# Kernel optimization log

Hardware: AMD Instinct MI355X
Metric: run time of the kernel (lower is better)

The kernel has to match this reference:

```python
import jax, jax.numpy as jnp
import numpy as np

EMBED_DIM = 1024
NUM_HEADS = 16
HEAD_DIM = EMBED_DIM // NUM_HEADS


def setup_inputs() -> dict:
    key = jax.random.key(0)
    ks = jax.random.split(key, 9)
    B, S, D = 2, 2048, EMBED_DIM
    scale = 1.0 / np.sqrt(D)
    x = jax.random.normal(ks[0], (B, S, D), dtype=jnp.float32)
    wq = jax.random.normal(ks[1], (D, D), dtype=jnp.float32) * scale
    bq = jax.random.normal(ks[2], (D,), dtype=jnp.float32) * 0.02
    wk = jax.random.normal(ks[3], (D, D), dtype=jnp.float32) * scale
    bk = jax.random.normal(ks[4], (D,), dtype=jnp.float32) * 0.02
    wv = jax.random.normal(ks[5], (D, D), dtype=jnp.float32) * scale
    bv = jax.random.normal(ks[6], (D,), dtype=jnp.float32) * 0.02
    wo = jax.random.normal(ks[7], (D, D), dtype=jnp.float32) * scale
    bo = jax.random.normal(ks[8], (D,), dtype=jnp.float32) * 0.02
    return {"x": x, "wq": wq, "bq": bq, "wk": wk, "bk": bk,
            "wv": wv, "bv": bv, "wo": wo, "bo": bo}


def reference(x, wq, bq, wk, bk, wv, bv, wo, bo):
    B, S, D = x.shape
    H, Hd = NUM_HEADS, HEAD_DIM
    # separate QKV linears (weights stored [in, out] so x @ w)
    q = (x @ wq + bq).reshape(B, S, H, Hd).transpose(0, 2, 1, 3)  # [B,H,S,Hd]
    k = (x @ wk + bk).reshape(B, S, H, Hd).transpose(0, 2, 1, 3)
    v = (x @ wv + bv).reshape(B, S, H, Hd).transpose(0, 2, 1, 3)
    scores = jnp.einsum('bhqd,bhkd->bhqk', q, k) / jnp.sqrt(jnp.float32(Hd))
    attn = jax.nn.softmax(scores, axis=-1)
    context = jnp.einsum('bhqk,bhkd->bhqd', attn, v)
    context = context.transpose(0, 2, 1, 3).reshape(B, S, D)
    return context @ wo + bo
```

## Files before the change

kernel.cpp:

```cpp
#include <hip/hip_runtime.h>
#include <cstdint>
#include <cstddef>


typedef float floatx4 __attribute__((ext_vector_type(4)));
typedef __bf16 bf16x8 __attribute__((ext_vector_type(8)));
union ABFrag { bf16x8 v; uint4 q; unsigned short u[8]; unsigned int w[4]; };

__device__ __forceinline__ unsigned short f2bf(float f) {
    unsigned int u = __builtin_bit_cast(unsigned int, f);
    return (unsigned short)((u + 0x7FFFu + ((u >> 16) & 1u)) >> 16);
}

__device__ __forceinline__ unsigned int pkbf(float lo, float hi) {
    unsigned int a = __builtin_bit_cast(unsigned int, hi) + 0x8000u;
    unsigned int b = __builtin_bit_cast(unsigned int, lo) + 0x8000u;
    return __builtin_amdgcn_perm(a, b, 0x07060302u);
}

#if __has_builtin(__builtin_amdgcn_exp2f)
#define EXP2F(x) __builtin_amdgcn_exp2f(x)
#else
#define EXP2F(x) exp2f(x)
#endif

__device__ __forceinline__ void glds16(const void* g, void* l) {
    __builtin_amdgcn_global_load_lds(
        (const __attribute__((address_space(1))) unsigned int*)(uintptr_t)g,
        (__attribute__((address_space(3))) unsigned int*)(unsigned int)(uintptr_t)l,
        16, 0, 0);
}

__global__ void convert_x_kernel(const float* __restrict__ x,
                                 unsigned short* __restrict__ xb) {
    int i = (blockIdx.x * 256 + threadIdx.x) * 8;
    float4 a = *(const float4*)(x + i);
    float4 b = *(const float4*)(x + i + 4);
    union { unsigned short u[8]; uint4 q; } o;
    o.u[0] = f2bf(a.x); o.u[1] = f2bf(a.y); o.u[2] = f2bf(a.z); o.u[3] = f2bf(a.w);
    o.u[4] = f2bf(b.x); o.u[5] = f2bf(b.y); o.u[6] = f2bf(b.z); o.u[7] = f2bf(b.w);
    *(uint4*)(xb + i) = o.q;
}

__global__ void convert_wT_kernel(const float* __restrict__ w0, const float* __restrict__ w1,
                                  const float* __restrict__ w2, const float* __restrict__ w3,
                                  unsigned short* __restrict__ wT) {
    __shared__ unsigned short t[32][40];
    const float* w = (blockIdx.z == 0) ? w0 : (blockIdx.z == 1) ? w1
                   : (blockIdx.z == 2) ? w2 : w3;
    unsigned short* dst = wT + (size_t)blockIdx.z * 1024 * 1024;
    const int k0 = blockIdx.x * 32, n0 = blockIdx.y * 32;
    const int tid = threadIdx.x;
    {
        int ry = tid >> 3, cx = (tid & 7) * 4;
        float4 v = *(const float4*)(w + (size_t)(k0 + ry) * 1024 + n0 + cx);
        t[cx + 0][ry] = f2bf(v.x); t[cx + 1][ry] = f2bf(v.y);
        t[cx + 2][ry] = f2bf(v.z); t[cx + 3][ry] = f2bf(v.w);
    }
    __syncthreads();
    int n = tid >> 3, kc = (tid & 7) * 4;
    *(uint2*)(dst + (size_t)(n0 + n) * 1024 + k0 + kc) = *(const uint2*)&t[n][kc];
}

template<int KIND>
__launch_bounds__(256, 2)
__global__ void gemm_kernel(const unsigned short* __restrict__ A,
                            const unsigned short* __restrict__ wT,
                            const float* __restrict__ bias0,
                            const float* __restrict__ bias1,
                            const float* __restrict__ bias2,
                            void* __restrict__ out0,
                            void* __restrict__ out1,
                            void* __restrict__ out2)
{
    __shared__ unsigned short a_s[128 * 32];
    __shared__ unsigned short b_s[128 * 32];

    const int tid  = threadIdx.x;
    const int wid  = tid >> 6;
    const int lane = tid & 63;
    const int quad = lane >> 4;
    const int l15  = lane & 15;
    const int wm   = (wid >> 1) * 64;
    const int wn   = (wid & 1) * 64;
    const int m0   = blockIdx.y * 128;
    const int n0   = blockIdx.x * 128;

    const unsigned short* Bt = (KIND == 0) ? wT + (size_t)blockIdx.z * (1024 * 1024) : wT;
    const float* bias = (KIND == 0)
        ? (blockIdx.z == 0 ? bias0 : blockIdx.z == 1 ? bias1 : bias2) : bias0;

    const int sr = lane >> 2;
    const int sc = (lane & 3) * 8;
    const unsigned short* gA = A  + (size_t)(m0 + wid * 32 + sr) * 1024 + sc;
    const unsigned short* gB = Bt + (size_t)(n0 + wid * 32 + sr) * 1024 + sc;
    unsigned short* lA = a_s + wid * 1024;
    unsigned short* lB = b_s + wid * 1024;

    floatx4 acc[4][4];
    #pragma unroll
    for (int i = 0; i < 4; i++)
        #pragma unroll
        for (int j = 0; j < 4; j++)
            acc[i][j] = floatx4{0.f, 0.f, 0.f, 0.f};

    for (int k0 = 0; k0 < 1024; k0 += 32) {
        __syncthreads();
        glds16(gA + k0,             lA);
        glds16(gA + k0 + 16 * 1024, lA + 512);
        glds16(gB + k0,             lB);
        glds16(gB + k0 + 16 * 1024, lB + 512);
        __syncthreads();

        ABFrag af[4], bf4[4];
        #pragma unroll
        for (int i = 0; i < 4; i++)
            af[i].q = *(const uint4*)(a_s + (wm + i * 16 + l15) * 32 + quad * 8);
        #pragma unroll
        for (int j = 0; j < 4; j++)
            bf4[j].q = *(const uint4*)(b_s + (wn + j * 16 + l15) * 32 + quad * 8);
        #pragma unroll
        for (int i = 0; i < 4; i++)
            #pragma unroll
            for (int j = 0; j < 4; j++)
                acc[i][j] = __builtin_amdgcn_mfma_f32_16x16x32_bf16(
                    af[i].v, bf4[j].v, acc[i][j], 0, 0, 0);
    }

    if constexpr (KIND == 1) {
        float* out = (float*)out0;
        #pragma unroll
        for (int j = 0; j < 4; j++) {
            int gn = n0 + wn + j * 16 + l15;
            float bval = bias[gn];
            #pragma unroll
            for (int i = 0; i < 4; i++)
                #pragma unroll
                for (int r = 0; r < 4; r++) {
                    int gm = m0 + wm + i * 16 + quad * 4 + r;
                    out[(size_t)gm * 1024 + gn] = acc[i][j][r] + bval;
                }
        }
    } else {
        if (blockIdx.z == 0) {
            const float SCQ = 0.125f * 1.44269504088896f;
            unsigned short* out = (unsigned short*)out0;
            #pragma unroll
            for (int j = 0; j < 4; j++) {
                int gn = n0 + wn + j * 16 + l15;
                float bval = bias[gn];
                int h = gn >> 6, d = gn & 63;
                #pragma unroll
                for (int i = 0; i < 4; i++)
                    #pragma unroll
                    for (int r = 0; r < 4; r++) {
                        int gm = m0 + wm + i * 16 + quad * 4 + r;
                        int b = gm >> 11, s = gm & 2047;
                        out[(((size_t)(b * 16 + h) * 2048 + s) << 6) + d] =
                            f2bf((acc[i][j][r] + bval) * SCQ);
                    }
            }
        } else if (blockIdx.z == 1) {
            unsigned short* out = (unsigned short*)out1;
            #pragma unroll
            for (int j = 0; j < 4; j++) {
                int gn = n0 + wn + j * 16 + l15;
                float bval = bias[gn];
                int h = gn >> 6, d = gn & 63;
                int dg = d >> 3, dl = d & 7;
                #pragma unroll
                for (int i = 0; i < 4; i++)
                    #pragma unroll
                    for (int r = 0; r < 4; r++) {
                        int gm = m0 + wm + i * 16 + quad * 4 + r;
                        int b = gm >> 11, s = gm & 2047;
                        int dphys = ((dg ^ (s & 7)) << 3) | dl;
                        out[(((size_t)(b * 16 + h) * 2048 + s) << 6) + dphys] =
                            f2bf(acc[i][j][r] + bval);
                    }
            }
        } else {
            __shared__ unsigned short t_s[128][136];
            #pragma unroll
            for (int j = 0; j < 4; j++) {
                int nl = wn + j * 16 + l15;
                float bval = bias[n0 + nl];
                #pragma unroll
                for (int i = 0; i < 4; i++)
                    #pragma unroll
                    for (int r = 0; r < 4; r++)
                        t_s[nl][wm + i * 16 + quad * 4 + r] = f2bf(acc[i][j][r] + bval);
            }
            __syncthreads();
            unsigned short* out = (unsigned short*)out2;
            const int n  = tid >> 1, half = tid & 1;
            const int bh = (m0 >> 11) * 16 + ((n0 + n) >> 6);
            const int d  = (n0 + n) & 63;
            const int chunk = ((m0 & 2047) >> 6) + half;
            const int dmask = d & 7;
            unsigned short* dstb = out + ((size_t)(bh * 32 + chunk) * 64 + d) * 64;
            const unsigned short* src = &t_s[n][half * 64];
            #pragma unroll
            for (int gp = 0; gp < 8; gp++) {
                int u1 = 32 * (gp >> 2) + 4 * (gp & 3);
                uint2 lo = *(const uint2*)(src + u1);
                uint2 hi = *(const uint2*)(src + u1 + 16);
                unsigned short* dq = dstb + ((gp ^ dmask) << 3);
                *(uint2*)dq       = lo;
                *(uint2*)(dq + 4) = hi;
            }
        }
    }
}

__launch_bounds__(256, 2)
__global__ void attn_kernel(const unsigned short* __restrict__ Q,
                            const unsigned short* __restrict__ K,
                            const unsigned short* __restrict__ Vt,
                            unsigned short* __restrict__ ctx)
{
    __shared__ unsigned short smem[2][2][4096];

    const int tid  = threadIdx.x;
    const int wid  = tid >> 6;
    const int lane = tid & 63;
    const int quad = lane >> 4;
    const int l15  = lane & 15;
    const int xr   = l15 & 7;

    const int bh = blockIdx.y;
    const unsigned short* Qh = Q + (size_t)bh * (2048 * 64);
    const char* Kc = (const char*)(K  + (size_t)bh * (2048 * 64));
    const char* Vc = (const char*)(Vt + (size_t)bh * (2048 * 64));
    const int q0 = blockIdx.x * 128 + wid * 32;

    ABFrag qf[2][2];
    #pragma unroll
    for (int jq = 0; jq < 2; jq++)
        #pragma unroll
        for (int s = 0; s < 2; s++)
            qf[jq][s].q = *(const uint4*)(Qh + (size_t)(q0 + jq * 16 + l15) * 64
                                          + s * 32 + quad * 8);

    int kcol[2], vcol[2];
    kcol[0] = ((quad    ) ^ xr) << 3;
    kcol[1] = ((quad + 4) ^ xr) << 3;
    vcol[0] = ((quad    ) ^ xr) << 3;
    vcol[1] = ((quad + 4) ^ xr) << 3;

    floatx4 acc[4][2];
    #pragma unroll
    for (int i = 0; i < 4; i++)
        #pragma unroll
        for (int jq = 0; jq < 2; jq++)
            acc[i][jq] = floatx4{0.f, 0.f, 0.f, 0.f};
    float lrun[2] = {0.f, 0.f};

    auto stage = [&](int c, int b) {
        const char* gk = Kc + (size_t)c * 8192 + wid * 2048 + lane * 16;
        char* lk = (char*)&smem[b][0][0] + wid * 2048;
        glds16(gk,        lk);
        glds16(gk + 1024, lk + 1024);
        const char* gv = Vc + (size_t)c * 8192 + wid * 2048 + lane * 16;
        char* lv = (char*)&smem[b][1][0] + wid * 2048;
        glds16(gv,        lv);
        glds16(gv + 1024, lv + 1024);
    };

    stage(0, 0);

    for (int c = 0; c < 32; ++c) {
        const int b = c & 1;
        __syncthreads();
        if (c + 1 < 32) stage(c + 1, b ^ 1);

        const unsigned short* ks = &smem[b][0][0];
        const unsigned short* vs = &smem[b][1][0];

        floatx4 st[4][2];
        #pragma unroll
        for (int kt = 0; kt < 4; kt++) {
            ABFrag k0, k1;
            const unsigned short* kr = ks + (kt * 16 + l15) * 64;
            k0.q = *(const uint4*)(kr + kcol[0]);
            k1.q = *(const uint4*)(kr + kcol[1]);
            #pragma unroll
            for (int jq = 0; jq < 2; jq++) {
                floatx4 t = floatx4{0.f, 0.f, 0.f, 0.f};
                t = __builtin_amdgcn_mfma_f32_16x16x32_bf16(k0.v, qf[jq][0].v, t, 0, 0, 0);
                t = __builtin_amdgcn_mfma_f32_16x16x32_bf16(k1.v, qf[jq][1].v, t, 0, 0, 0);
                st[kt][jq] = t;
            }
        }

        unsigned int pk[4][2][2];
        #pragma unroll
        for (int jq = 0; jq < 2; jq++) {
            float ls = 0.f;
            #pragma unroll
            for (int kt = 0; kt < 4; kt++) {
                #pragma unroll
                for (int t2 = 0; t2 < 2; t2++) {
                    float p0 = EXP2F(st[kt][jq][2 * t2 + 0]);
                    float p1 = EXP2F(st[kt][jq][2 * t2 + 1]);
                    ls += p0 + p1;
                    pk[kt][jq][t2] = pkbf(p0, p1);
                }
            }
            lrun[jq] += ls;
        }

        #pragma unroll
        for (int s2 = 0; s2 < 2; s2++) {
            ABFrag pf[2];
            #pragma unroll
            for (int jq = 0; jq < 2; jq++) {
                pf[jq].w[0] = pk[2 * s2 + 0][jq][0];
                pf[jq].w[1] = pk[2 * s2 + 0][jq][1];
                pf[jq].w[2] = pk[2 * s2 + 1][jq][0];
                pf[jq].w[3] = pk[2 * s2 + 1][jq][1];
            }
            #pragma unroll
            for (int i = 0; i < 4; i++) {
                ABFrag vf;
                vf.q = *(const uint4*)(vs + (i * 16 + l15) * 64 + vcol[s2]);
                #pragma unroll
                for (int jq = 0; jq < 2; jq++)
                    acc[i][jq] = __builtin_amdgcn_mfma_f32_16x16x32_bf16(
                        vf.v, pf[jq].v, acc[i][jq], 0, 0, 0);
            }
        }
    }

    const int b_ = bh >> 4, h = bh & 15;
    #pragma unroll
    for (int jq = 0; jq < 2; jq++) {
        float s = lrun[jq];
        s += __shfl_xor(s, 16, 64);
        s += __shfl_xor(s, 32, 64);
        float inv = 1.0f / s;
        int q = q0 + jq * 16 + l15;
        size_t base = (size_t)(b_ * 2048 + q) * 1024 + h * 64;
        #pragma unroll
        for (int i = 0; i < 4; i++) {
            float v0 = acc[i][jq][0] * inv, v1 = acc[i][jq][1] * inv;
            float v2 = acc[i][jq][2] * inv, v3 = acc[i][jq][3] * inv;
            uint2 w2 = make_uint2(pkbf(v0, v1), pkbf(v2, v3));
            *(uint2*)(ctx + base + i * 16 + quad * 4) = w2;
        }
    }
}

extern "C" void kernel_launch(void* const* d_in, const int* in_sizes, int n_in,
                              void* d_out, int out_size, void* d_ws, size_t ws_size,
                              hipStream_t stream)
{
    const float* x  = (const float*)d_in[0];
    const float* wq = (const float*)d_in[1];
    const float* bq = (const float*)d_in[2];
    const float* wk = (const float*)d_in[3];
    const float* bk = (const float*)d_in[4];
    const float* wv = (const float*)d_in[5];
    const float* bv = (const float*)d_in[6];
    const float* wo = (const float*)d_in[7];
    const float* bo = (const float*)d_in[8];

    const size_t NE = (size_t)4096 * 1024;
    unsigned short* xb  = (unsigned short*)d_ws;
    unsigned short* wT  = xb  + NE;
    unsigned short* qb  = wT  + NE;
    unsigned short* kb  = qb  + NE;
    unsigned short* vtb = kb  + NE;
    unsigned short* ctx = vtb + NE;

    hipLaunchKernelGGL(convert_x_kernel, dim3(2048), dim3(256), 0, stream, x, xb);
    hipLaunchKernelGGL(convert_wT_kernel, dim3(32, 32, 4), dim3(256), 0, stream,
                       wq, wk, wv, wo, wT);
    hipLaunchKernelGGL((gemm_kernel<0>), dim3(8, 32, 3), dim3(256), 0, stream,
                       xb, wT, bq, bk, bv, (void*)qb, (void*)kb, (void*)vtb);
    hipLaunchKernelGGL(attn_kernel, dim3(16, 32), dim3(256), 0, stream, qb, kb, vtb, ctx);
    hipLaunchKernelGGL((gemm_kernel<1>), dim3(8, 32), dim3(256), 0, stream,
                       ctx, wT + 3 * NE / 4, bo, nullptr, nullptr, d_out, nullptr, nullptr);
}
```

Measured before the change: 198.0 us.

## Split attention KV range across two wave groups with LDS reduction

Doubles the attention block to 512 threads. Two groups of four waves each process half of the key/value sequence for the same query tile, with separate double-buffered LDS staging. The partial output accumulators and row sums are combined through shared memory at the end before normalisation and the store. This is meant to raise occupancy and latency hiding by halving each wave's serial loop. In exchange it adds a reduction step and doubles LDS use per block.

```diff
diff --git a/kernel.cpp b/kernel.cpp
--- a/kernel.cpp
+++ b/kernel.cpp
@@ -213,16 +213,18 @@
     }
 }
 
-__launch_bounds__(256, 2)
+__launch_bounds__(512, 4)
 __global__ void attn_kernel(const unsigned short* __restrict__ Q,
                             const unsigned short* __restrict__ K,
                             const unsigned short* __restrict__ Vt,
                             unsigned short* __restrict__ ctx)
 {
-    __shared__ unsigned short smem[2][2][4096];
+    __shared__ unsigned short smem[2][2][2][4096];
 
     const int tid  = threadIdx.x;
     const int wid  = tid >> 6;
+    const int kh   = wid >> 2;
+    const int wq   = wid & 3;
     const int lane = tid & 63;
     const int quad = lane >> 4;
     const int l15  = lane & 15;
@@ -230,9 +232,9 @@
 
     const int bh = blockIdx.y;
     const unsigned short* Qh = Q + (size_t)bh * (2048 * 64);
-    const char* Kc = (const char*)(K  + (size_t)bh * (2048 * 64));
-    const char* Vc = (const char*)(Vt + (size_t)bh * (2048 * 64));
-    const int q0 = blockIdx.x * 128 + wid * 32;
+    const char* Kc = (const char*)(K  + (size_t)bh * (2048 * 64)) + (size_t)kh * (16 * 8192);
+    const char* Vc = (const char*)(Vt + (size_t)bh * (2048 * 64)) + (size_t)kh * (16 * 8192);
+    const int q0 = blockIdx.x * 128 + wq * 32;
 
     ABFrag qf[2][2];
     #pragma unroll
@@ -242,11 +244,9 @@
             qf[jq][s].q = *(const uint4*)(Qh + (size_t)(q0 + jq * 16 + l15) * 64
                                           + s * 32 + quad * 8);
 
-    int kcol[2], vcol[2];
+    int kcol[2];
     kcol[0] = ((quad    ) ^ xr) << 3;
     kcol[1] = ((quad + 4) ^ xr) << 3;
-    vcol[0] = ((quad    ) ^ xr) << 3;
-    vcol[1] = ((quad + 4) ^ xr) << 3;
 
     floatx4 acc[4][2];
     #pragma unroll
@@ -257,25 +257,25 @@
     float lrun[2] = {0.f, 0.f};
 
     auto stage = [&](int c, int b) {
-        const char* gk = Kc + (size_t)c * 8192 + wid * 2048 + lane * 16;
-        char* lk = (char*)&smem[b][0][0] + wid * 2048;
+        const char* gk = Kc + (size_t)c * 8192 + wq * 2048 + lane * 16;
+        char* lk = (char*)&smem[b][kh][0][0] + wq * 2048;
         glds16(gk,        lk);
         glds16(gk + 1024, lk + 1024);
-        const char* gv = Vc + (size_t)c * 8192 + wid * 2048 + lane * 16;
-        char* lv = (char*)&smem[b][1][0] + wid * 2048;
+        const char* gv = Vc + (size_t)c * 8192 + wq * 2048 + lane * 16;
+        char* lv = (char*)&smem[b][kh][1][0] + wq * 2048;
         glds16(gv,        lv);
         glds16(gv + 1024, lv + 1024);
     };
 
     stage(0, 0);
 
-    for (int c = 0; c < 32; ++c) {
+    for (int c = 0; c < 16; ++c) {
         const int b = c & 1;
         __syncthreads();
-        if (c + 1 < 32) stage(c + 1, b ^ 1);
-
-        const unsigned short* ks = &smem[b][0][0];
-        const unsigned short* vs = &smem[b][1][0];
+        if (c + 1 < 16) stage(c + 1, b ^ 1);
+
+        const unsigned short* ks = &smem[b][kh][0][0];
+        const unsigned short* vs = &smem[b][kh][1][0];
 
         floatx4 st[4][2];
         #pragma unroll
@@ -323,7 +323,7 @@
             #pragma unroll
             for (int i = 0; i < 4; i++) {
                 ABFrag vf;
-                vf.q = *(const uint4*)(vs + (i * 16 + l15) * 64 + vcol[s2]);
+                vf.q = *(const uint4*)(vs + (i * 16 + l15) * 64 + kcol[s2]);
                 #pragma unroll
                 for (int jq = 0; jq < 2; jq++)
                     acc[i][jq] = __builtin_amdgcn_mfma_f32_16x16x32_bf16(
@@ -332,21 +332,44 @@
         }
     }
 
-    const int b_ = bh >> 4, h = bh & 15;
-    #pragma unroll
-    for (int jq = 0; jq < 2; jq++) {
-        float s = lrun[jq];
-        s += __shfl_xor(s, 16, 64);
-        s += __shfl_xor(s, 32, 64);
-        float inv = 1.0f / s;
-        int q = q0 + jq * 16 + l15;
-        size_t base = (size_t)(b_ * 2048 + q) * 1024 + h * 64;
-        #pragma unroll
-        for (int i = 0; i < 4; i++) {
-            float v0 = acc[i][jq][0] * inv, v1 = acc[i][jq][1] * inv;
-            float v2 = acc[i][jq][2] * inv, v3 = acc[i][jq][3] * inv;
-            uint2 w2 = make_uint2(pkbf(v0, v1), pkbf(v2, v3));
-            *(uint2*)(ctx + base + i * 16 + quad * 4) = w2;
+    __syncthreads();
+    float* sf = (float*)&smem[0][0][0][0];
+    float* myp = sf + (size_t)(wq * 64 + lane) * 40;
+    if (kh) {
+        #pragma unroll
+        for (int i = 0; i < 4; i++)
+            #pragma unroll
+            for (int jq = 0; jq < 2; jq++)
+                *(floatx4*)(myp + (i * 2 + jq) * 4) = acc[i][jq];
+        myp[32] = lrun[0];
+        myp[33] = lrun[1];
+    }
+    __syncthreads();
+    if (!kh) {
+        #pragma unroll
+        for (int i = 0; i < 4; i++)
+            #pragma unroll
+            for (int jq = 0; jq < 2; jq++)
+                acc[i][jq] += *(const floatx4*)(myp + (i * 2 + jq) * 4);
+        lrun[0] += myp[32];
+        lrun[1] += myp[33];
+
+        const int b_ = bh >> 4, h = bh & 15;
+        #pragma unroll
+        for (int jq = 0; jq < 2; jq++) {
+            float s = lrun[jq];
+            s += __shfl_xor(s, 16, 64);
+            s += __shfl_xor(s, 32, 64);
+            float inv = 1.0f / s;
+            int q = q0 + jq * 16 + l15;
+            size_t base = (size_t)(b_ * 2048 + q) * 1024 + h * 64;
+            #pragma unroll
+            for (int i = 0; i < 4; i++) {
+                float v0 = acc[i][jq][0] * inv, v1 = acc[i][jq][1] * inv;
+                float v2 = acc[i][jq][2] * inv, v3 = acc[i][jq][3] * inv;
+                uint2 w2 = make_uint2(pkbf(v0, v1), pkbf(v2, v3));
+                *(uint2*)(ctx + base + i * 16 + quad * 4) = w2;
+            }
         }
     }
 }
@@ -378,7 +401,7 @@
                        wq, wk, wv, wo, wT);
     hipLaunchKernelGGL((gemm_kernel<0>), dim3(8, 32, 3), dim3(256), 0, stream,
                        xb, wT, bq, bk, bv, (void*)qb, (void*)kb, (void*)vtb);
-    hipLaunchKernelGGL(attn_kernel, dim3(16, 32), dim3(256), 0, stream, qb, kb, vtb, ctx);
+    hipLaunchKernelGGL(attn_kernel, dim3(16, 32), dim3(512), 0, stream, qb, kb, vtb, ctx);
     hipLaunchKernelGGL((gemm_kernel<1>), dim3(8, 32), dim3(256), 0, stream,
                        ctx, wT + 3 * NE / 4, bo, nullptr, nullptr, d_out, nullptr, nullptr);
 }
```

Result: no change. 197.4 us (-0.3%).
